# Optimization experiments

Hardware: AMD Instinct MI355X
Metric: run time of the kernel (lower is better)

## Reference

```python
import jax, jax.numpy as jnp
import numpy as np

N_NODES = 50000
N_EDGES = 800000
N_GRAPHS = 512
NODE_DIM, EDGE_DIM, HID, OUT = 96, 16, 128, 128


def _gine_conv(x, src, dst, edge_attr, We, be, W1, b1, W2, b2, eps=0.0):
    # messages: ReLU(x_j + Lin_edge(edge_attr)), gathered at source nodes
    msg = jax.nn.relu(x[src] + edge_attr @ We + be)          # [E, d]
    agg = jax.ops.segment_sum(msg, dst, num_segments=N_NODES)  # [N, d]
    h = (1.0 + eps) * x + agg
    # GIN MLP: Linear -> ReLU -> Linear
    return jax.nn.relu(h @ W1 + b1) @ W2 + b2


def setup_inputs() -> dict:
    key = jax.random.key(0)
    ks = jax.random.split(key, 16)
    x = jax.random.normal(ks[0], (N_NODES, NODE_DIM), jnp.float32)
    edge_index = jax.random.randint(ks[1], (2, N_EDGES), 0, N_NODES, jnp.int32)
    edge_attr = jax.random.normal(ks[2], (N_EDGES, EDGE_DIM), jnp.float32)
    batch = jnp.sort(jax.random.randint(ks[3], (N_NODES,), 0, N_GRAPHS, jnp.int32))

    def lin(k, fi, fo):
        s = 1.0 / np.sqrt(fi)
        kw, kb = jax.random.split(k)
        return (jax.random.uniform(kw, (fi, fo), jnp.float32, -s, s),
                jax.random.uniform(kb, (fo,), jnp.float32, -s, s))

    We1, be1 = lin(ks[4], EDGE_DIM, NODE_DIM)
    W1a, b1a = lin(ks[5], NODE_DIM, HID)
    W1b, b1b = lin(ks[6], HID, HID)
    We2, be2 = lin(ks[7], EDGE_DIM, HID)
    W2a, b2a = lin(ks[8], HID, HID)
    W2b, b2b = lin(ks[9], HID, HID)
    Wfc, bfc = lin(ks[10], HID, OUT)
    return {"x": x, "edge_index": edge_index, "edge_attr": edge_attr, "batch": batch,
            "We1": We1, "be1": be1, "W1a": W1a, "b1a": b1a, "W1b": W1b, "b1b": b1b,
            "We2": We2, "be2": be2, "W2a": W2a, "b2a": b2a, "W2b": W2b, "b2b": b2b,
            "Wfc": Wfc, "bfc": bfc}


def reference(x, edge_index, edge_attr, batch,
              We1, be1, W1a, b1a, W1b, b1b,
              We2, be2, W2a, b2a, W2b, b2b,
              Wfc, bfc):
    src, dst = edge_index[0], edge_index[1]
    h = jax.nn.relu(_gine_conv(x, src, dst, edge_attr, We1, be1, W1a, b1a, W1b, b1b))
    h = jax.nn.relu(_gine_conv(h, src, dst, edge_attr, We2, be2, W2a, b2a, W2b, b2b))
    pooled = jax.ops.segment_sum(h, batch, num_segments=N_GRAPHS)  # [G, HID]
    return pooled @ Wfc + bfc
```

## Files before the change

kernel.cpp:

```cpp
#include <hip/hip_runtime.h>
#include <hip/hip_bf16.h>

#define N_NODES 50000
#define N_EDGES 800000
#define N_GRAPHS 512
#define CAP 48

typedef __attribute__((ext_vector_type(8))) short short8v;
typedef __attribute__((ext_vector_type(4))) float f32x4;

__device__ inline float bf2f(unsigned short u) {
    union { unsigned int i; float f; } v; v.i = ((unsigned int)u) << 16; return v.f;
}
__device__ inline short f2bf(float f) {
    __hip_bfloat16 h = __float2bfloat16(f);
    return *reinterpret_cast<short*>(&h);
}


__global__ __launch_bounds__(256) void fill_csr(
    const int* __restrict__ dst, const int* __restrict__ src,
    int* __restrict__ deg, int2* __restrict__ ecsr)
{
    int e = blockIdx.x * blockDim.x + threadIdx.x;
    if (e < N_EDGES) {
        int d = dst[e];
        int slot = atomicAdd(&deg[d], 1);
        if (slot < CAP) ecsr[d * CAP + slot] = make_int2(e, src[e]);
    }
}

template <int DIN>
__global__ __launch_bounds__(256) void cvt_perm_kernel(
    const float* __restrict__ in, unsigned int* __restrict__ out, int total)
{
    int t = blockIdx.x * blockDim.x + threadIdx.x;
    if (t < total) {
        const int m2 = t % (DIN / 2);
        const int n  = t / (DIN / 2);
        const int p  = m2 >> 4;
        const int c  = m2 & 15;
        const float lo = in[(size_t)n * DIN + 32 * p + c];
        const float hi = in[(size_t)n * DIN + 32 * p + 16 + c];
        out[t] = (unsigned int)(unsigned short)f2bf(lo) |
                 ((unsigned int)(unsigned short)f2bf(hi) << 16);
    }
}

template <int K>
__global__ __launch_bounds__(256) void cvtT_kernel(
    const float* __restrict__ W, unsigned short* __restrict__ WT)
{
    int t = blockIdx.x * blockDim.x + threadIdx.x;
    if (t < 128 * K) {
        const int d = t / K;
        const int k = t % K;
        WT[t] = (unsigned short)f2bf(W[k * 128 + d]);
    }
}

template <int DIN>
__global__ __launch_bounds__(256, 8) void gather_v6(
    const unsigned short* __restrict__ hin,
    const float* __restrict__ ea,
    const int* __restrict__ deg,
    const int2* __restrict__ ecsr,
    const float* __restrict__ We,
    const float* __restrict__ be,
    unsigned short* __restrict__ hpre)
{
    constexpr int NB = DIN / 16;
    constexpr int NP = DIN / 32;

    const int lane = threadIdx.x & 63;
    const int col = lane & 15;
    const int grp = lane >> 4;
    const int gwave = (blockIdx.x * blockDim.x + threadIdx.x) >> 6;
    const int nwaves = (gridDim.x * blockDim.x) >> 6;

    short8v Bf[NB];
#pragma unroll
    for (int b = 0; b < NB; ++b) {
        short8v f = {};
        if (grp < 2) {
#pragma unroll
            for (int j = 0; j < 8; ++j)
                f[j] = f2bf(We[(grp * 8 + j) * DIN + b * 16 + col]);
        } else if (grp == 2) {
            f[0] = f2bf(be[b * 16 + col]);
        }
        Bf[b] = f;
    }

    for (int n = gwave; n < N_NODES; n += nwaves) {
        const int dgc = min(deg[n], CAP);
        const int nch = (dgc + 15) >> 4;

        float accv[NB];
#pragma unroll
        for (int b = 0; b < NB; ++b) accv[b] = 0.0f;

        for (int c = 0; c < nch; ++c) {
            const int base = n * CAP + c * 16;
            const int vc = dgc - c * 16;

            int e_l = 0, s_l = 0;
            if (lane < vc) {
                const int2 pr = ecsr[base + lane];
                e_l = pr.x;
                s_l = pr.y;
            }

            const int e_col = __shfl(e_l, col);
            short8v Af = {};
            if (grp < 2) {
                if (col < vc) {
                    const float* ap = ea + (size_t)e_col * 16 + grp * 8;
                    const float4 a0 = *(const float4*)(ap);
                    const float4 a1 = *(const float4*)(ap + 4);
                    Af[0] = f2bf(a0.x); Af[1] = f2bf(a0.y);
                    Af[2] = f2bf(a0.z); Af[3] = f2bf(a0.w);
                    Af[4] = f2bf(a1.x); Af[5] = f2bf(a1.y);
                    Af[6] = f2bf(a1.z); Af[7] = f2bf(a1.w);
                }
            } else if (grp == 2) {
                Af[0] = (short)0x3F80;
            }

            int sid[4];
#pragma unroll
            for (int r = 0; r < 4; ++r) sid[r] = __shfl(s_l, 4 * grp + r);

#pragma unroll
            for (int p = 0; p < NP; ++p) {
                const f32x4 zero = {0.0f, 0.0f, 0.0f, 0.0f};
                f32x4 lin0 = __builtin_amdgcn_mfma_f32_16x16x32_bf16(Af, Bf[2 * p], zero, 0, 0, 0);
                f32x4 lin1 = __builtin_amdgcn_mfma_f32_16x16x32_bf16(Af, Bf[2 * p + 1], zero, 0, 0, 0);
                float part0 = 0.0f, part1 = 0.0f;
#pragma unroll
                for (int r = 0; r < 4; ++r) {
                    if (4 * grp + r < vc) {
                        const unsigned int u = *(const unsigned int*)
                            (hin + (size_t)sid[r] * DIN + 32 * p + 2 * col);
                        const float xlo = bf2f((unsigned short)(u & 0xffffu));
                        const float xhi = bf2f((unsigned short)(u >> 16));
                        part0 += fmaxf(xlo + lin0[r], 0.0f);
                        part1 += fmaxf(xhi + lin1[r], 0.0f);
                    }
                }
                part0 += __shfl_xor(part0, 16);
                part0 += __shfl_xor(part0, 32);
                part1 += __shfl_xor(part1, 16);
                part1 += __shfl_xor(part1, 32);
                accv[2 * p] += part0;
                accv[2 * p + 1] += part1;
            }
        }

        if (lane < 16) {
#pragma unroll
            for (int p = 0; p < NP; ++p) {
                const unsigned int u = *(const unsigned int*)
                    (hin + (size_t)n * DIN + 32 * p + 2 * lane);
                const float lo = bf2f((unsigned short)(u & 0xffffu)) + accv[2 * p];
                const float hi = bf2f((unsigned short)(u >> 16)) + accv[2 * p + 1];
                *(unsigned int*)(hpre + (size_t)n * DIN + 32 * p + 2 * lane) =
                    (unsigned int)(unsigned short)f2bf(lo) |
                    ((unsigned int)(unsigned short)f2bf(hi) << 16);
            }
        }
    }
}

template <int DIN, int MODE>
__global__ __launch_bounds__(256) void mlp_mfma(
    const unsigned short* __restrict__ hpre,
    const unsigned short* __restrict__ WaT,
    const float* __restrict__ ba,
    const unsigned short* __restrict__ WbT,
    const float* __restrict__ bb,
    unsigned short* __restrict__ h1out,
    const int* __restrict__ batch,
    float* __restrict__ pooled)
{
    constexpr int KS1 = DIN / 32;
    __shared__ unsigned short hls[32][DIN + 8];
    __shared__ unsigned short uls[32][128 + 8];
    __shared__ float vls[(MODE == 1) ? 32 : 1][(MODE == 1) ? 132 : 1];

    const int n0 = blockIdx.x * 32;
    const int tid = threadIdx.x;

    for (int f = tid * 4; f < 32 * DIN; f += 1024) {
        const int row = f / DIN, colc = f % DIN;
        const int n = n0 + row;
        ushort4 u = make_ushort4(0, 0, 0, 0);
        if (n < N_NODES) u = *(const ushort4*)(hpre + (size_t)n * DIN + colc);
        const int p = colc >> 5;
        const int q = (colc & 31) >> 2;
        hls[row][32 * p + 2 * q]          = u.x;
        hls[row][32 * p + 16 + 2 * q]     = u.y;
        hls[row][32 * p + 2 * q + 1]      = u.z;
        hls[row][32 * p + 16 + 2 * q + 1] = u.w;
    }
    __syncthreads();

    const int lane = tid & 63;
    const int w = tid >> 6;
    const int col = lane & 15;
    const int grp = lane >> 4;

    f32x4 acc00 = {0,0,0,0}, acc01 = {0,0,0,0}, acc10 = {0,0,0,0}, acc11 = {0,0,0,0};
#pragma unroll
    for (int ks = 0; ks < KS1; ++ks) {
        const short8v A0 = *(const short8v*)&hls[col][ks * 32 + grp * 8];
        const short8v A1 = *(const short8v*)&hls[16 + col][ks * 32 + grp * 8];
        const short8v B0 = *(const short8v*)&WaT[(size_t)(2 * w * 16 + col) * DIN + ks * 32 + grp * 8];
        const short8v B1 = *(const short8v*)&WaT[(size_t)((2 * w + 1) * 16 + col) * DIN + ks * 32 + grp * 8];
        acc00 = __builtin_amdgcn_mfma_f32_16x16x32_bf16(A0, B0, acc00, 0, 0, 0);
        acc01 = __builtin_amdgcn_mfma_f32_16x16x32_bf16(A0, B1, acc01, 0, 0, 0);
        acc10 = __builtin_amdgcn_mfma_f32_16x16x32_bf16(A1, B0, acc10, 0, 0, 0);
        acc11 = __builtin_amdgcn_mfma_f32_16x16x32_bf16(A1, B1, acc11, 0, 0, 0);
    }
    const float ba0 = ba[2 * w * 16 + col];
    const float ba1 = ba[(2 * w + 1) * 16 + col];
#pragma unroll
    for (int i = 0; i < 4; ++i) {
        const int r0 = grp * 4 + i;
        uls[r0][2 * w * 16 + col]            = (unsigned short)f2bf(fmaxf(acc00[i] + ba0, 0.f));
        uls[r0][(2 * w + 1) * 16 + col]      = (unsigned short)f2bf(fmaxf(acc01[i] + ba1, 0.f));
        uls[16 + r0][2 * w * 16 + col]       = (unsigned short)f2bf(fmaxf(acc10[i] + ba0, 0.f));
        uls[16 + r0][(2 * w + 1) * 16 + col] = (unsigned short)f2bf(fmaxf(acc11[i] + ba1, 0.f));
    }
    __syncthreads();

    acc00 = (f32x4){0,0,0,0}; acc01 = (f32x4){0,0,0,0};
    acc10 = (f32x4){0,0,0,0}; acc11 = (f32x4){0,0,0,0};
#pragma unroll
    for (int ks = 0; ks < 4; ++ks) {
        const short8v A0 = *(const short8v*)&uls[col][ks * 32 + grp * 8];
        const short8v A1 = *(const short8v*)&uls[16 + col][ks * 32 + grp * 8];
        const short8v B0 = *(const short8v*)&WbT[(size_t)(2 * w * 16 + col) * 128 + ks * 32 + grp * 8];
        const short8v B1 = *(const short8v*)&WbT[(size_t)((2 * w + 1) * 16 + col) * 128 + ks * 32 + grp * 8];
        acc00 = __builtin_amdgcn_mfma_f32_16x16x32_bf16(A0, B0, acc00, 0, 0, 0);
        acc01 = __builtin_amdgcn_mfma_f32_16x16x32_bf16(A0, B1, acc01, 0, 0, 0);
        acc10 = __builtin_amdgcn_mfma_f32_16x16x32_bf16(A1, B0, acc10, 0, 0, 0);
        acc11 = __builtin_amdgcn_mfma_f32_16x16x32_bf16(A1, B1, acc11, 0, 0, 0);
    }
    const float bb0 = bb[2 * w * 16 + col];
    const float bb1 = bb[(2 * w + 1) * 16 + col];

    if (MODE == 0) {
#pragma unroll
        for (int i = 0; i < 4; ++i) {
            const int nA = n0 + grp * 4 + i;
            if (nA < N_NODES) {
                const float v0 = fmaxf(acc00[i] + bb0, 0.f);
                const float v1 = fmaxf(acc01[i] + bb1, 0.f);
                *(unsigned int*)(h1out + (size_t)nA * 128 + 32 * w + 2 * col) =
                    (unsigned int)(unsigned short)f2bf(v0) |
                    ((unsigned int)(unsigned short)f2bf(v1) << 16);
            }
            const int nB = n0 + 16 + grp * 4 + i;
            if (nB < N_NODES) {
                const float v0 = fmaxf(acc10[i] + bb0, 0.f);
                const float v1 = fmaxf(acc11[i] + bb1, 0.f);
                *(unsigned int*)(h1out + (size_t)nB * 128 + 32 * w + 2 * col) =
                    (unsigned int)(unsigned short)f2bf(v0) |
                    ((unsigned int)(unsigned short)f2bf(v1) << 16);
            }
        }
    } else {
#pragma unroll
        for (int i = 0; i < 4; ++i) {
            const int r0 = grp * 4 + i;
            vls[r0][2 * w * 16 + col]            = fmaxf(acc00[i] + bb0, 0.f);
            vls[r0][(2 * w + 1) * 16 + col]      = fmaxf(acc01[i] + bb1, 0.f);
            vls[16 + r0][2 * w * 16 + col]       = fmaxf(acc10[i] + bb0, 0.f);
            vls[16 + r0][(2 * w + 1) * 16 + col] = fmaxf(acc11[i] + bb1, 0.f);
        }
        __syncthreads();
        if (tid < 128) {
            const int d = tid;
            const int lim = min(32, N_NODES - n0);
            float s = 0.0f;
            int bprev = -1;
            for (int q = 0; q < lim; ++q) {
                const int b = batch[n0 + q];
                if (b != bprev) {
                    if (bprev >= 0) atomicAdd(&pooled[bprev * 128 + d], s);
                    s = 0.0f;
                    bprev = b;
                }
                s += vls[q][d];
            }
            if (bprev >= 0) atomicAdd(&pooled[bprev * 128 + d], s);
        }
    }
}

__global__ __launch_bounds__(128) void fc_kernel(
    const float* __restrict__ pooled,
    const float* __restrict__ Wfc,
    const float* __restrict__ bfc,
    float* __restrict__ out)
{
    const int g = blockIdx.x;
    const int d = threadIdx.x;
    __shared__ float sp[128];
    sp[d] = pooled[g * 128 + d];
    __syncthreads();
    float acc = bfc[d];
    for (int k = 0; k < 128; ++k) acc = fmaf(sp[k], Wfc[k * 128 + d], acc);
    out[g * 128 + d] = acc;
}

extern "C" void kernel_launch(void* const* d_in, const int* in_sizes, int n_in,
                              void* d_out, int out_size, void* d_ws, size_t ws_size,
                              hipStream_t stream) {
    const float* x    = (const float*)d_in[0];
    const int*   eidx = (const int*)d_in[1];
    const float* ea   = (const float*)d_in[2];
    const int*   batch= (const int*)d_in[3];
    const float* We1  = (const float*)d_in[4];
    const float* be1  = (const float*)d_in[5];
    const float* W1a  = (const float*)d_in[6];
    const float* b1a  = (const float*)d_in[7];
    const float* W1b  = (const float*)d_in[8];
    const float* b1b  = (const float*)d_in[9];
    const float* We2  = (const float*)d_in[10];
    const float* be2  = (const float*)d_in[11];
    const float* W2a  = (const float*)d_in[12];
    const float* b2a  = (const float*)d_in[13];
    const float* W2b  = (const float*)d_in[14];
    const float* b2b  = (const float*)d_in[15];
    const float* Wfc  = (const float*)d_in[16];
    const float* bfc  = (const float*)d_in[17];
    float* out = (float*)d_out;

    const int* srcp = eidx;
    const int* dstp = eidx + N_EDGES;

    char* w = (char*)d_ws;
    unsigned short* hpre = (unsigned short*)w;  w += (size_t)N_NODES * 128 * 2;
    unsigned short* h1 = (unsigned short*)w;    w += (size_t)N_NODES * 128 * 2;
    int* deg  = (int*)w;                        w += (size_t)N_NODES * 4;
    int2* ecsr = (int2*)w;                      w += (size_t)N_NODES * CAP * 8;
    float* pooled = (float*)w;                  w += (size_t)N_GRAPHS * 128 * 4;
    unsigned short* W1aT = (unsigned short*)w;  w += (size_t)128 * 96 * 2;
    unsigned short* W1bT = (unsigned short*)w;  w += (size_t)128 * 128 * 2;
    unsigned short* W2aT = (unsigned short*)w;  w += (size_t)128 * 128 * 2;
    unsigned short* W2bT = (unsigned short*)w;  w += (size_t)128 * 128 * 2;

    unsigned short* x16 = h1;

    hipMemsetAsync(deg, 0, (size_t)N_NODES * 4, stream);
    fill_csr<<<(N_EDGES + 255) / 256, 256, 0, stream>>>(dstp, srcp, deg, ecsr);
    {
        const int total = N_NODES * 96 / 2;
        cvt_perm_kernel<96><<<(total + 255) / 256, 256, 0, stream>>>(
            x, (unsigned int*)x16, total);
    }
    cvtT_kernel<96><<<(128 * 96 + 255) / 256, 256, 0, stream>>>(W1a, W1aT);
    cvtT_kernel<128><<<(128 * 128 + 255) / 256, 256, 0, stream>>>(W1b, W1bT);
    cvtT_kernel<128><<<(128 * 128 + 255) / 256, 256, 0, stream>>>(W2a, W2aT);
    cvtT_kernel<128><<<(128 * 128 + 255) / 256, 256, 0, stream>>>(W2b, W2bT);

    const int gblocks = 2048;
    const int mblocks = (N_NODES + 31) / 32;

    gather_v6<96><<<gblocks, 256, 0, stream>>>(
        x16, ea, deg, ecsr, We1, be1, hpre);
    mlp_mfma<96, 0><<<mblocks, 256, 0, stream>>>(
        hpre, W1aT, b1a, W1bT, b1b, h1, nullptr, nullptr);

    gather_v6<128><<<gblocks, 256, 0, stream>>>(
        h1, ea, deg, ecsr, We2, be2, hpre);
    hipMemsetAsync(pooled, 0, (size_t)N_GRAPHS * 128 * 4, stream);
    mlp_mfma<128, 1><<<mblocks, 256, 0, stream>>>(
        hpre, W2aT, b2a, W2bT, b2b, nullptr, batch, pooled);

    fc_kernel<<<N_GRAPHS, 128, 0, stream>>>(pooled, Wfc, bfc, out);
}
```

Before: 377.2 us.

## Build compact CSR with pre-sorted bf16 edge attributes for gather

Replaces the fixed-capacity padded CSR (int2 edge id and src per slot) with a compact CSR built by degree count, atomic base assignment and scatter. Edge attributes are converted to bf16 and stored contiguously in destination order, and source ids are stored as 16-bit values, so the gather reads the attributes sequentially instead of randomly from fp32. The cross-lane shuffle reduction is moved out of the per-chunk loop to run once per node. This adds three preprocessing kernels and an extra write of the edge attributes, keeps the old path as a fallback when the workspace is too small, and relies on the node count fitting in 16 bits.

```diff
diff --git a/kernel.cpp b/kernel.cpp
--- a/kernel.cpp
+++ b/kernel.cpp
@@ -18,15 +18,41 @@
 }
 
 
-__global__ __launch_bounds__(256) void fill_csr(
+__global__ __launch_bounds__(256) void count_deg(
+    const int* __restrict__ dst, int* __restrict__ deg)
+{
+    int e = blockIdx.x * blockDim.x + threadIdx.x;
+    if (e < N_EDGES) atomicAdd(&deg[dst[e]], 1);
+}
+
+__global__ __launch_bounds__(256) void assign_base(
+    const int* __restrict__ deg, int* __restrict__ basep, int* __restrict__ counter)
+{
+    int n = blockIdx.x * blockDim.x + threadIdx.x;
+    if (n < N_NODES) basep[n] = atomicAdd(counter, deg[n]);
+}
+
+__global__ __launch_bounds__(256) void scatter_edges(
     const int* __restrict__ dst, const int* __restrict__ src,
-    int* __restrict__ deg, int2* __restrict__ ecsr)
+    const float* __restrict__ ea,
+    const int* __restrict__ basep, int* __restrict__ fill,
+    unsigned short* __restrict__ srcdst, unsigned short* __restrict__ eadst)
 {
     int e = blockIdx.x * blockDim.x + threadIdx.x;
     if (e < N_EDGES) {
-        int d = dst[e];
-        int slot = atomicAdd(&deg[d], 1);
-        if (slot < CAP) ecsr[d * CAP + slot] = make_int2(e, src[e]);
+        const int d = dst[e];
+        const int slot = atomicAdd(&fill[d], 1);
+        const size_t pos = (size_t)basep[d] + slot;
+        srcdst[pos] = (unsigned short)src[e];
+        const float4* ap = (const float4*)(ea + (size_t)e * 16);
+        const float4 a0 = ap[0], a1 = ap[1], a2 = ap[2], a3 = ap[3];
+        short8v o0, o1;
+        o0[0] = f2bf(a0.x); o0[1] = f2bf(a0.y); o0[2] = f2bf(a0.z); o0[3] = f2bf(a0.w);
+        o0[4] = f2bf(a1.x); o0[5] = f2bf(a1.y); o0[6] = f2bf(a1.z); o0[7] = f2bf(a1.w);
+        o1[0] = f2bf(a2.x); o1[1] = f2bf(a2.y); o1[2] = f2bf(a2.z); o1[3] = f2bf(a2.w);
+        o1[4] = f2bf(a3.x); o1[5] = f2bf(a3.y); o1[6] = f2bf(a3.z); o1[7] = f2bf(a3.w);
+        ((short8v*)eadst)[2 * pos]     = o0;
+        ((short8v*)eadst)[2 * pos + 1] = o1;
     }
 }
 
@@ -56,6 +82,123 @@
         const int d = t / K;
         const int k = t % K;
         WT[t] = (unsigned short)f2bf(W[k * 128 + d]);
+    }
+}
+
+__global__ __launch_bounds__(256) void fill_csr(
+    const int* __restrict__ dst, const int* __restrict__ src,
+    int* __restrict__ deg, int2* __restrict__ ecsr)
+{
+    int e = blockIdx.x * blockDim.x + threadIdx.x;
+    if (e < N_EDGES) {
+        int d = dst[e];
+        int slot = atomicAdd(&deg[d], 1);
+        if (slot < CAP) ecsr[d * CAP + slot] = make_int2(e, src[e]);
+    }
+}
+
+template <int DIN>
+__global__ __launch_bounds__(256, 8) void gather_v7(
+    const unsigned short* __restrict__ hin,
+    const unsigned short* __restrict__ srcdst,
+    const unsigned short* __restrict__ eadst,
+    const int* __restrict__ deg,
+    const int* __restrict__ basep,
+    const float* __restrict__ We,
+    const float* __restrict__ be,
+    unsigned short* __restrict__ hpre)
+{
+    constexpr int NB = DIN / 16;
+    constexpr int NP = DIN / 32;
+
+    const int lane = threadIdx.x & 63;
+    const int col = lane & 15;
+    const int grp = lane >> 4;
+    const int gwave = (blockIdx.x * blockDim.x + threadIdx.x) >> 6;
+    const int nwaves = (gridDim.x * blockDim.x) >> 6;
+
+    short8v Bf[NB];
+#pragma unroll
+    for (int b = 0; b < NB; ++b) {
+        short8v f = {};
+        if (grp < 2) {
+#pragma unroll
+            for (int j = 0; j < 8; ++j)
+                f[j] = f2bf(We[(grp * 8 + j) * DIN + b * 16 + col]);
+        } else if (grp == 2) {
+            f[0] = f2bf(be[b * 16 + col]);
+        }
+        Bf[b] = f;
+    }
+
+    for (int n = gwave; n < N_NODES; n += nwaves) {
+        const int dgc = deg[n];
+        const int nch = (dgc + 15) >> 4;
+        const int b0 = basep[n];
+
+        float accv[NB];
+#pragma unroll
+        for (int b = 0; b < NB; ++b) accv[b] = 0.0f;
+
+        for (int c = 0; c < nch; ++c) {
+            const int pos0 = b0 + 16 * c;
+            const int vcc = min(dgc - 16 * c, 16);
+
+            int s_l = 0;
+            if (lane < vcc) s_l = srcdst[pos0 + lane];
+
+            short8v Af = {};
+            if (grp < 2) {
+                if (col < vcc)
+                    Af = *(const short8v*)(eadst + (size_t)(pos0 + col) * 16 + grp * 8);
+            } else if (grp == 2) {
+                Af[0] = (short)0x3F80;
+            }
+
+            int sid[4];
+#pragma unroll
+            for (int r = 0; r < 4; ++r) sid[r] = __shfl(s_l, 4 * grp + r);
+
+#pragma unroll
+            for (int p = 0; p < NP; ++p) {
+                const f32x4 zero = {0.0f, 0.0f, 0.0f, 0.0f};
+                f32x4 lin0 = __builtin_amdgcn_mfma_f32_16x16x32_bf16(Af, Bf[2 * p], zero, 0, 0, 0);
+                f32x4 lin1 = __builtin_amdgcn_mfma_f32_16x16x32_bf16(Af, Bf[2 * p + 1], zero, 0, 0, 0);
+                float part0 = 0.0f, part1 = 0.0f;
+#pragma unroll
+                for (int r = 0; r < 4; ++r) {
+                    if (4 * grp + r < vcc) {
+                        const unsigned int u = *(const unsigned int*)
+                            (hin + (size_t)sid[r] * DIN + 32 * p + 2 * col);
+                        const float xlo = bf2f((unsigned short)(u & 0xffffu));
+                        const float xhi = bf2f((unsigned short)(u >> 16));
+                        part0 += fmaxf(xlo + lin0[r], 0.0f);
+                        part1 += fmaxf(xhi + lin1[r], 0.0f);
+                    }
+                }
+                accv[2 * p]     += part0;
+                accv[2 * p + 1] += part1;
+            }
+        }
+
+#pragma unroll
+        for (int b = 0; b < NB; ++b) {
+            accv[b] += __shfl_xor(accv[b], 16);
+            accv[b] += __shfl_xor(accv[b], 32);
+        }
+
+        if (lane < 16) {
+#pragma unroll
+            for (int p = 0; p < NP; ++p) {
+                const unsigned int u = *(const unsigned int*)
+                    (hin + (size_t)n * DIN + 32 * p + 2 * lane);
+                const float lo = bf2f((unsigned short)(u & 0xffffu)) + accv[2 * p];
+                const float hi = bf2f((unsigned short)(u >> 16)) + accv[2 * p + 1];
+                *(unsigned int*)(hpre + (size_t)n * DIN + 32 * p + 2 * lane) =
+                    (unsigned int)(unsigned short)f2bf(lo) |
+                    ((unsigned int)(unsigned short)f2bf(hi) << 16);
+            }
+        }
     }
 }
 
@@ -148,13 +291,15 @@
                         part1 += fmaxf(xhi + lin1[r], 0.0f);
                     }
                 }
-                part0 += __shfl_xor(part0, 16);
-                part0 += __shfl_xor(part0, 32);
-                part1 += __shfl_xor(part1, 16);
-                part1 += __shfl_xor(part1, 32);
-                accv[2 * p] += part0;
+                accv[2 * p]     += part0;
                 accv[2 * p + 1] += part1;
             }
+        }
+
+#pragma unroll
+        for (int b = 0; b < NB; ++b) {
+            accv[b] += __shfl_xor(accv[b], 16);
+            accv[b] += __shfl_xor(accv[b], 32);
         }
 
         if (lane < 16) {
@@ -341,44 +486,99 @@
     const int* srcp = eidx;
     const int* dstp = eidx + N_EDGES;
 
-    char* w = (char*)d_ws;
-    unsigned short* hpre = (unsigned short*)w;  w += (size_t)N_NODES * 128 * 2;
-    unsigned short* h1 = (unsigned short*)w;    w += (size_t)N_NODES * 128 * 2;
-    int* deg  = (int*)w;                        w += (size_t)N_NODES * 4;
-    int2* ecsr = (int2*)w;                      w += (size_t)N_NODES * CAP * 8;
-    float* pooled = (float*)w;                  w += (size_t)N_GRAPHS * 128 * 4;
-    unsigned short* W1aT = (unsigned short*)w;  w += (size_t)128 * 96 * 2;
-    unsigned short* W1bT = (unsigned short*)w;  w += (size_t)128 * 128 * 2;
-    unsigned short* W2aT = (unsigned short*)w;  w += (size_t)128 * 128 * 2;
-    unsigned short* W2bT = (unsigned short*)w;  w += (size_t)128 * 128 * 2;
-
-    unsigned short* x16 = h1;
-
-    hipMemsetAsync(deg, 0, (size_t)N_NODES * 4, stream);
-    fill_csr<<<(N_EDGES + 255) / 256, 256, 0, stream>>>(dstp, srcp, deg, ecsr);
-    {
-        const int total = N_NODES * 96 / 2;
-        cvt_perm_kernel<96><<<(total + 255) / 256, 256, 0, stream>>>(
-            x, (unsigned int*)x16, total);
-    }
-    cvtT_kernel<96><<<(128 * 96 + 255) / 256, 256, 0, stream>>>(W1a, W1aT);
-    cvtT_kernel<128><<<(128 * 128 + 255) / 256, 256, 0, stream>>>(W1b, W1bT);
-    cvtT_kernel<128><<<(128 * 128 + 255) / 256, 256, 0, stream>>>(W2a, W2aT);
-    cvtT_kernel<128><<<(128 * 128 + 255) / 256, 256, 0, stream>>>(W2b, W2bT);
-
     const int gblocks = 2048;
     const int mblocks = (N_NODES + 31) / 32;
 
-    gather_v6<96><<<gblocks, 256, 0, stream>>>(
-        x16, ea, deg, ecsr, We1, be1, hpre);
-    mlp_mfma<96, 0><<<mblocks, 256, 0, stream>>>(
-        hpre, W1aT, b1a, W1bT, b1b, h1, nullptr, nullptr);
-
-    gather_v6<128><<<gblocks, 256, 0, stream>>>(
-        h1, ea, deg, ecsr, We2, be2, hpre);
-    hipMemsetAsync(pooled, 0, (size_t)N_GRAPHS * 128 * 4, stream);
-    mlp_mfma<128, 1><<<mblocks, 256, 0, stream>>>(
-        hpre, W2aT, b2a, W2bT, b2b, nullptr, batch, pooled);
-
-    fc_kernel<<<N_GRAPHS, 128, 0, stream>>>(pooled, Wfc, bfc, out);
-}
+    {
+        char* w = (char*)d_ws;
+        unsigned short* bufA = (unsigned short*)w;  w += (size_t)N_NODES * 128 * 2;
+        unsigned short* bufB = (unsigned short*)w;  w += (size_t)N_NODES * 128 * 2;
+        int* deg   = (int*)w;                       w += (size_t)N_NODES * 4;
+        int* basep = (int*)w;                       w += (size_t)N_NODES * 4;
+        int* fillp = (int*)w;                       w += (size_t)N_NODES * 4;
+        int* counter = (int*)w;                     w += 256;
+        unsigned short* srcdst = (unsigned short*)w; w += (size_t)N_EDGES * 2;
+        unsigned short* eadst = (unsigned short*)w;  w += (size_t)N_EDGES * 16 * 2;
+        float* pooled = (float*)w;                  w += (size_t)N_GRAPHS * 128 * 4;
+        unsigned short* W1aT = (unsigned short*)w;  w += (size_t)128 * 96 * 2;
+        unsigned short* W1bT = (unsigned short*)w;  w += (size_t)128 * 128 * 2;
+        unsigned short* W2aT = (unsigned short*)w;  w += (size_t)128 * 128 * 2;
+        unsigned short* W2bT = (unsigned short*)w;  w += (size_t)128 * 128 * 2;
+        const size_t need = (size_t)(w - (char*)d_ws);
+
+        if (ws_size >= need) {
+            unsigned short* x16 = bufB;
+
+            hipMemsetAsync(deg, 0, (size_t)N_NODES * 4, stream);
+            hipMemsetAsync(fillp, 0, (size_t)N_NODES * 4, stream);
+            hipMemsetAsync(counter, 0, 4, stream);
+            count_deg<<<(N_EDGES + 255) / 256, 256, 0, stream>>>(dstp, deg);
+            assign_base<<<(N_NODES + 255) / 256, 256, 0, stream>>>(deg, basep, counter);
+            scatter_edges<<<(N_EDGES + 255) / 256, 256, 0, stream>>>(
+                dstp, srcp, ea, basep, fillp, srcdst, eadst);
+            {
+                const int total = N_NODES * 96 / 2;
+                cvt_perm_kernel<96><<<(total + 255) / 256, 256, 0, stream>>>(
+                    x, (unsigned int*)x16, total);
+            }
+            cvtT_kernel<96><<<(128 * 96 + 255) / 256, 256, 0, stream>>>(W1a, W1aT);
+            cvtT_kernel<128><<<(128 * 128 + 255) / 256, 256, 0, stream>>>(W1b, W1bT);
+            cvtT_kernel<128><<<(128 * 128 + 255) / 256, 256, 0, stream>>>(W2a, W2aT);
+            cvtT_kernel<128><<<(128 * 128 + 255) / 256, 256, 0, stream>>>(W2b, W2bT);
+
+            gather_v7<96><<<gblocks, 256, 0, stream>>>(
+                x16, srcdst, eadst, deg, basep, We1, be1, bufA);
+            mlp_mfma<96, 0><<<mblocks, 256, 0, stream>>>(
+                bufA, W1aT, b1a, W1bT, b1b, bufB, nullptr, nullptr);
+
+            gather_v7<128><<<gblocks, 256, 0, stream>>>(
+                bufB, srcdst, eadst, deg, basep, We2, be2, bufA);
+            hipMemsetAsync(pooled, 0, (size_t)N_GRAPHS * 128 * 4, stream);
+            mlp_mfma<128, 1><<<mblocks, 256, 0, stream>>>(
+                bufA, W2aT, b2a, W2bT, b2b, nullptr, batch, pooled);
+
+            fc_kernel<<<N_GRAPHS, 128, 0, stream>>>(pooled, Wfc, bfc, out);
+            return;
+        }
+    }
+
+    {
+        char* w = (char*)d_ws;
+        unsigned short* hpre = (unsigned short*)w;  w += (size_t)N_NODES * 128 * 2;
+        unsigned short* h1 = (unsigned short*)w;    w += (size_t)N_NODES * 128 * 2;
+        int* deg  = (int*)w;                        w += (size_t)N_NODES * 4;
+        int2* ecsr = (int2*)w;                      w += (size_t)N_NODES * CAP * 8;
+        float* pooled = (float*)w;                  w += (size_t)N_GRAPHS * 128 * 4;
+        unsigned short* W1aT = (unsigned short*)w;  w += (size_t)128 * 96 * 2;
+        unsigned short* W1bT = (unsigned short*)w;  w += (size_t)128 * 128 * 2;
+        unsigned short* W2aT = (unsigned short*)w;  w += (size_t)128 * 128 * 2;
+        unsigned short* W2bT = (unsigned short*)w;  w += (size_t)128 * 128 * 2;
+
+        unsigned short* x16 = h1;
+
+        hipMemsetAsync(deg, 0, (size_t)N_NODES * 4, stream);
+        fill_csr<<<(N_EDGES + 255) / 256, 256, 0, stream>>>(dstp, srcp, deg, ecsr);
+        {
+            const int total = N_NODES * 96 / 2;
+            cvt_perm_kernel<96><<<(total + 255) / 256, 256, 0, stream>>>(
+                x, (unsigned int*)x16, total);
+        }
+        cvtT_kernel<96><<<(128 * 96 + 255) / 256, 256, 0, stream>>>(W1a, W1aT);
+        cvtT_kernel<128><<<(128 * 128 + 255) / 256, 256, 0, stream>>>(W1b, W1bT);
+        cvtT_kernel<128><<<(128 * 128 + 255) / 256, 256, 0, stream>>>(W2a, W2aT);
+        cvtT_kernel<128><<<(128 * 128 + 255) / 256, 256, 0, stream>>>(W2b, W2bT);
+
+        gather_v6<96><<<gblocks, 256, 0, stream>>>(
+            x16, ea, deg, ecsr, We1, be1, hpre);
+        mlp_mfma<96, 0><<<mblocks, 256, 0, stream>>>(
+            hpre, W1aT, b1a, W1bT, b1b, h1, nullptr, nullptr);
+
+        gather_v6<128><<<gblocks, 256, 0, stream>>>(
+            h1, ea, deg, ecsr, We2, be2, hpre);
+        hipMemsetAsync(pooled, 0, (size_t)N_GRAPHS * 128 * 4, stream);
+        mlp_mfma<128, 1><<<mblocks, 256, 0, stream>>>(
+            hpre, W2aT, b2a, W2bT, b2b, nullptr, batch, pooled);
+
+        fc_kernel<<<N_GRAPHS, 128, 0, stream>>>(pooled, Wfc, bfc, out);
+    }
+}
```

New measurement: 369.9 us. No clear change (-2.0%).

## Build compact CSR with pre-sorted bf16 edge attributes and defer lane reductions

Applied to the files above, without the earlier changes.

Replaces the fixed-capacity padded edge table with a compact per-node layout built by degree count, atomic base assignment and scatter. Source ids are stored as 16-bit and edge attributes are pre-converted to bf16 in destination order, so the gather streams contiguous attributes instead of doing random fp32 loads. Cross-lane shuffle reductions move out of the per-chunk loop to once per node, and the small conversion kernels are merged into one launch. This adds three preprocessing launches plus atomic base allocation, and it removes the CAP truncation of high-degree nodes. The 16-bit source ids only hold because node count is below 65536.

```diff
diff --git a/kernel.cpp b/kernel.cpp
--- a/kernel.cpp
+++ b/kernel.cpp
@@ -4,7 +4,6 @@
 #define N_NODES 50000
 #define N_EDGES 800000
 #define N_GRAPHS 512
-#define CAP 48
 
 typedef __attribute__((ext_vector_type(8))) short short8v;
 typedef __attribute__((ext_vector_type(4))) float f32x4;
@@ -18,53 +17,85 @@
 }
 
 
-__global__ __launch_bounds__(256) void fill_csr(
+__global__ __launch_bounds__(256) void count_deg(
+    const int* __restrict__ dst, int* __restrict__ deg)
+{
+    int e = blockIdx.x * blockDim.x + threadIdx.x;
+    if (e < N_EDGES) atomicAdd(&deg[dst[e]], 1);
+}
+
+__global__ __launch_bounds__(256) void assign_base(
+    const int* __restrict__ deg, int* __restrict__ basep, int* __restrict__ counter)
+{
+    int n = blockIdx.x * blockDim.x + threadIdx.x;
+    if (n < N_NODES) basep[n] = atomicAdd(counter, deg[n]);
+}
+
+__global__ __launch_bounds__(256) void scatter_edges(
     const int* __restrict__ dst, const int* __restrict__ src,
-    int* __restrict__ deg, int2* __restrict__ ecsr)
+    const float* __restrict__ ea,
+    const int* __restrict__ basep, int* __restrict__ fill,
+    unsigned short* __restrict__ srcdst, unsigned short* __restrict__ eadst)
 {
     int e = blockIdx.x * blockDim.x + threadIdx.x;
     if (e < N_EDGES) {
-        int d = dst[e];
-        int slot = atomicAdd(&deg[d], 1);
-        if (slot < CAP) ecsr[d * CAP + slot] = make_int2(e, src[e]);
-    }
-}
-
-template <int DIN>
-__global__ __launch_bounds__(256) void cvt_perm_kernel(
-    const float* __restrict__ in, unsigned int* __restrict__ out, int total)
+        const int d = dst[e];
+        const int slot = atomicAdd(&fill[d], 1);
+        const size_t pos = (size_t)basep[d] + slot;
+        srcdst[pos] = (unsigned short)src[e];
+        const float4* ap = (const float4*)(ea + (size_t)e * 16);
+        const float4 a0 = ap[0], a1 = ap[1], a2 = ap[2], a3 = ap[3];
+        short8v o0, o1;
+        o0[0] = f2bf(a0.x); o0[1] = f2bf(a0.y); o0[2] = f2bf(a0.z); o0[3] = f2bf(a0.w);
+        o0[4] = f2bf(a1.x); o0[5] = f2bf(a1.y); o0[6] = f2bf(a1.z); o0[7] = f2bf(a1.w);
+        o1[0] = f2bf(a2.x); o1[1] = f2bf(a2.y); o1[2] = f2bf(a2.z); o1[3] = f2bf(a2.w);
+        o1[4] = f2bf(a3.x); o1[5] = f2bf(a3.y); o1[6] = f2bf(a3.z); o1[7] = f2bf(a3.w);
+        ((short8v*)eadst)[2 * pos]     = o0;
+        ((short8v*)eadst)[2 * pos + 1] = o1;
+    }
+}
+
+#define T0_CVT (N_NODES * 48)
+__global__ __launch_bounds__(256) void prep_convert(
+    const float* __restrict__ x,
+    const float* __restrict__ W1a, const float* __restrict__ W1b,
+    const float* __restrict__ W2a, const float* __restrict__ W2b,
+    unsigned int* __restrict__ x16,
+    unsigned short* __restrict__ W1aT, unsigned short* __restrict__ W1bT,
+    unsigned short* __restrict__ W2aT, unsigned short* __restrict__ W2bT)
 {
     int t = blockIdx.x * blockDim.x + threadIdx.x;
-    if (t < total) {
-        const int m2 = t % (DIN / 2);
-        const int n  = t / (DIN / 2);
+    if (t < T0_CVT) {
+        const int m2 = t % 48;
+        const int n  = t / 48;
         const int p  = m2 >> 4;
         const int c  = m2 & 15;
-        const float lo = in[(size_t)n * DIN + 32 * p + c];
-        const float hi = in[(size_t)n * DIN + 32 * p + 16 + c];
-        out[t] = (unsigned int)(unsigned short)f2bf(lo) |
+        const float lo = x[(size_t)n * 96 + 32 * p + c];
+        const float hi = x[(size_t)n * 96 + 32 * p + 16 + c];
+        x16[t] = (unsigned int)(unsigned short)f2bf(lo) |
                  ((unsigned int)(unsigned short)f2bf(hi) << 16);
-    }
-}
-
-template <int K>
-__global__ __launch_bounds__(256) void cvtT_kernel(
-    const float* __restrict__ W, unsigned short* __restrict__ WT)
-{
-    int t = blockIdx.x * blockDim.x + threadIdx.x;
-    if (t < 128 * K) {
-        const int d = t / K;
-        const int k = t % K;
-        WT[t] = (unsigned short)f2bf(W[k * 128 + d]);
-    }
+        return;
+    }
+    int u = t - T0_CVT;
+    if (u < 128 * 96) {
+        W1aT[u] = (unsigned short)f2bf(W1a[(u % 96) * 128 + u / 96]);
+        return;
+    }
+    u -= 128 * 96;
+    if (u < 16384) { W1bT[u] = (unsigned short)f2bf(W1b[(u & 127) * 128 + (u >> 7)]); return; }
+    u -= 16384;
+    if (u < 16384) { W2aT[u] = (unsigned short)f2bf(W2a[(u & 127) * 128 + (u >> 7)]); return; }
+    u -= 16384;
+    if (u < 16384) { W2bT[u] = (unsigned short)f2bf(W2b[(u & 127) * 128 + (u >> 7)]); }
 }
 
 template <int DIN>
-__global__ __launch_bounds__(256, 8) void gather_v6(
+__global__ __launch_bounds__(256, 8) void gather_v8(
     const unsigned short* __restrict__ hin,
-    const float* __restrict__ ea,
+    const unsigned short* __restrict__ srcdst,
+    const unsigned short* __restrict__ eadst,
     const int* __restrict__ deg,
-    const int2* __restrict__ ecsr,
+    const int* __restrict__ basep,
     const float* __restrict__ We,
     const float* __restrict__ be,
     unsigned short* __restrict__ hpre)
@@ -93,36 +124,25 @@
     }
 
     for (int n = gwave; n < N_NODES; n += nwaves) {
-        const int dgc = min(deg[n], CAP);
+        const int dgc = deg[n];
         const int nch = (dgc + 15) >> 4;
+        const int b0 = basep[n];
 
         float accv[NB];
 #pragma unroll
         for (int b = 0; b < NB; ++b) accv[b] = 0.0f;
 
         for (int c = 0; c < nch; ++c) {
-            const int base = n * CAP + c * 16;
-            const int vc = dgc - c * 16;
-
-            int e_l = 0, s_l = 0;
-            if (lane < vc) {
-                const int2 pr = ecsr[base + lane];
-                e_l = pr.x;
-                s_l = pr.y;
-            }
-
-            const int e_col = __shfl(e_l, col);
+            const int pos0 = b0 + 16 * c;
+            const int vcc = min(dgc - 16 * c, 16);
+
+            int s_l = 0;
+            if (lane < vcc) s_l = srcdst[pos0 + lane];
+
             short8v Af = {};
             if (grp < 2) {
-                if (col < vc) {
-                    const float* ap = ea + (size_t)e_col * 16 + grp * 8;
-                    const float4 a0 = *(const float4*)(ap);
-                    const float4 a1 = *(const float4*)(ap + 4);
-                    Af[0] = f2bf(a0.x); Af[1] = f2bf(a0.y);
-                    Af[2] = f2bf(a0.z); Af[3] = f2bf(a0.w);
-                    Af[4] = f2bf(a1.x); Af[5] = f2bf(a1.y);
-                    Af[6] = f2bf(a1.z); Af[7] = f2bf(a1.w);
-                }
+                if (col < vcc)
+                    Af = *(const short8v*)(eadst + (size_t)(pos0 + col) * 16 + grp * 8);
             } else if (grp == 2) {
                 Af[0] = (short)0x3F80;
             }
@@ -139,7 +159,7 @@
                 float part0 = 0.0f, part1 = 0.0f;
 #pragma unroll
                 for (int r = 0; r < 4; ++r) {
-                    if (4 * grp + r < vc) {
+                    if (4 * grp + r < vcc) {
                         const unsigned int u = *(const unsigned int*)
                             (hin + (size_t)sid[r] * DIN + 32 * p + 2 * col);
                         const float xlo = bf2f((unsigned short)(u & 0xffffu));
@@ -148,26 +168,38 @@
                         part1 += fmaxf(xhi + lin1[r], 0.0f);
                     }
                 }
-                part0 += __shfl_xor(part0, 16);
-                part0 += __shfl_xor(part0, 32);
-                part1 += __shfl_xor(part1, 16);
-                part1 += __shfl_xor(part1, 32);
-                accv[2 * p] += part0;
+                accv[2 * p]     += part0;
                 accv[2 * p + 1] += part1;
             }
         }
 
-        if (lane < 16) {
-#pragma unroll
-            for (int p = 0; p < NP; ++p) {
-                const unsigned int u = *(const unsigned int*)
-                    (hin + (size_t)n * DIN + 32 * p + 2 * lane);
-                const float lo = bf2f((unsigned short)(u & 0xffffu)) + accv[2 * p];
-                const float hi = bf2f((unsigned short)(u >> 16)) + accv[2 * p + 1];
-                *(unsigned int*)(hpre + (size_t)n * DIN + 32 * p + 2 * lane) =
-                    (unsigned int)(unsigned short)f2bf(lo) |
-                    ((unsigned int)(unsigned short)f2bf(hi) << 16);
-            }
+#pragma unroll
+        for (int b = 0; b < NB; ++b) {
+            accv[b] += __shfl_xor(accv[b], 16);
+            accv[b] += __shfl_xor(accv[b], 32);
+        }
+
+        const float t0l = __shfl(accv[0], col), t0h = __shfl(accv[1], col);
+        const float t1l = __shfl(accv[2], col), t1h = __shfl(accv[3], col);
+        const float t2l = __shfl(accv[4], col), t2h = __shfl(accv[5], col);
+        float lo, hi;
+        if (DIN == 128) {
+            const float t3l = __shfl(accv[NB - 2], col), t3h = __shfl(accv[NB - 1], col);
+            lo = (grp == 0) ? t0l : (grp == 1) ? t1l : (grp == 2) ? t2l : t3l;
+            hi = (grp == 0) ? t0h : (grp == 1) ? t1h : (grp == 2) ? t2h : t3h;
+        } else {
+            lo = (grp == 0) ? t0l : (grp == 1) ? t1l : t2l;
+            hi = (grp == 0) ? t0h : (grp == 1) ? t1h : t2h;
+        }
+
+        if (lane < DIN / 2) {
+            const unsigned int u =
+                ((const unsigned int*)(hin + (size_t)n * DIN))[lane];
+            const float slo = bf2f((unsigned short)(u & 0xffffu)) + lo;
+            const float shi = bf2f((unsigned short)(u >> 16)) + hi;
+            ((unsigned int*)(hpre + (size_t)n * DIN))[lane] =
+                (unsigned int)(unsigned short)f2bf(slo) |
+                ((unsigned int)(unsigned short)f2bf(shi) << 16);
         }
     }
 }
@@ -341,44 +373,49 @@
     const int* srcp = eidx;
     const int* dstp = eidx + N_EDGES;
 
+    const int gblocks = 2048;
+    const int mblocks = (N_NODES + 31) / 32;
+
     char* w = (char*)d_ws;
-    unsigned short* hpre = (unsigned short*)w;  w += (size_t)N_NODES * 128 * 2;
-    unsigned short* h1 = (unsigned short*)w;    w += (size_t)N_NODES * 128 * 2;
-    int* deg  = (int*)w;                        w += (size_t)N_NODES * 4;
-    int2* ecsr = (int2*)w;                      w += (size_t)N_NODES * CAP * 8;
+    unsigned short* bufA = (unsigned short*)w;  w += (size_t)N_NODES * 128 * 2;
+    unsigned short* bufB = (unsigned short*)w;  w += (size_t)N_NODES * 128 * 2;
+    int* deg   = (int*)w;                       w += (size_t)N_NODES * 4;
+    int* basep = (int*)w;                       w += (size_t)N_NODES * 4;
+    int* fillp = (int*)w;                       w += (size_t)N_NODES * 4;
+    int* counter = (int*)w;                     w += 256;
+    unsigned short* srcdst = (unsigned short*)w; w += (size_t)N_EDGES * 2;
+    unsigned short* eadst = (unsigned short*)w;  w += (size_t)N_EDGES * 16 * 2;
     float* pooled = (float*)w;                  w += (size_t)N_GRAPHS * 128 * 4;
     unsigned short* W1aT = (unsigned short*)w;  w += (size_t)128 * 96 * 2;
     unsigned short* W1bT = (unsigned short*)w;  w += (size_t)128 * 128 * 2;
     unsigned short* W2aT = (unsigned short*)w;  w += (size_t)128 * 128 * 2;
     unsigned short* W2bT = (unsigned short*)w;  w += (size_t)128 * 128 * 2;
 
-    unsigned short* x16 = h1;
+    unsigned short* x16 = bufB;
 
     hipMemsetAsync(deg, 0, (size_t)N_NODES * 4, stream);
-    fill_csr<<<(N_EDGES + 255) / 256, 256, 0, stream>>>(dstp, srcp, deg, ecsr);
+    hipMemsetAsync(fillp, 0, (size_t)N_NODES * 4, stream);
+    hipMemsetAsync(counter, 0, 4, stream);
+    count_deg<<<(N_EDGES + 255) / 256, 256, 0, stream>>>(dstp, deg);
+    assign_base<<<(N_NODES + 255) / 256, 256, 0, stream>>>(deg, basep, counter);
+    scatter_edges<<<(N_EDGES + 255) / 256, 256, 0, stream>>>(
+        dstp, srcp, ea, basep, fillp, srcdst, eadst);
     {
-        const int total = N_NODES * 96 / 2;
-        cvt_perm_kernel<96><<<(total + 255) / 256, 256, 0, stream>>>(
-            x, (unsigned int*)x16, total);
-    }
-    cvtT_kernel<96><<<(128 * 96 + 255) / 256, 256, 0, stream>>>(W1a, W1aT);
-    cvtT_kernel<128><<<(128 * 128 + 255) / 256, 256, 0, stream>>>(W1b, W1bT);
-    cvtT_kernel<128><<<(128 * 128 + 255) / 256, 256, 0, stream>>>(W2a, W2aT);
-    cvtT_kernel<128><<<(128 * 128 + 255) / 256, 256, 0, stream>>>(W2b, W2bT);
-
-    const int gblocks = 2048;
-    const int mblocks = (N_NODES + 31) / 32;
-
-    gather_v6<96><<<gblocks, 256, 0, stream>>>(
-        x16, ea, deg, ecsr, We1, be1, hpre);
+        const int total = T0_CVT + 128 * 96 + 3 * 16384;
+        prep_convert<<<(total + 255) / 256, 256, 0, stream>>>(
+            x, W1a, W1b, W2a, W2b, (unsigned int*)x16, W1aT, W1bT, W2aT, W2bT);
+    }
+
+    gather_v8<96><<<gblocks, 256, 0, stream>>>(
+        x16, srcdst, eadst, deg, basep, We1, be1, bufA);
     mlp_mfma<96, 0><<<mblocks, 256, 0, stream>>>(
-        hpre, W1aT, b1a, W1bT, b1b, h1, nullptr, nullptr);
-
-    gather_v6<128><<<gblocks, 256, 0, stream>>>(
-        h1, ea, deg, ecsr, We2, be2, hpre);
+        bufA, W1aT, b1a, W1bT, b1b, bufB, nullptr, nullptr);
+
+    gather_v8<128><<<gblocks, 256, 0, stream>>>(
+        bufB, srcdst, eadst, deg, basep, We2, be2, bufA);
     hipMemsetAsync(pooled, 0, (size_t)N_GRAPHS * 128 * 4, stream);
     mlp_mfma<128, 1><<<mblocks, 256, 0, stream>>>(
-        hpre, W2aT, b2a, W2bT, b2b, nullptr, batch, pooled);
+        bufA, W2aT, b2a, W2bT, b2b, nullptr, batch, pooled);
 
     fc_kernel<<<N_GRAPHS, 128, 0, stream>>>(pooled, Wfc, bfc, out);
 }
```

Measured after the change: 369.4 us. 1.02x faster.
